# Optimization experiments

Measured on AMD Instinct MI355X. Metric: run time of the kernel, lower is better.

The kernel has to match this reference:

```python
import jax, jax.numpy as jnp
import numpy as np

B, CIN, H, W = 32, 512, 16, 16
COUT, HEADS, SPARSITY = 2048, 8, 7
D = COUT // HEADS  # 256, must equal H*W
N = H * W


def conv1x1(x, w, b):
    # x: [B,C,H,W], w: [O,C], b: [O]
    return jnp.einsum('bchw,oc->bohw', x, w) + b[None, :, None, None]


def setup_inputs() -> dict:
    key = jax.random.key(0)
    ks = jax.random.split(key, 11)
    def lin(k, o, c):
        bound = 1.0 / np.sqrt(c)
        kw, kb = jax.random.split(k)
        return (jax.random.uniform(kw, (o, c), jnp.float32, -bound, bound),
                jax.random.uniform(kb, (o,), jnp.float32, -bound, bound))
    Wq, bq = lin(ks[0], COUT, CIN)
    Wk, bk = lin(ks[1], COUT, CIN)
    Wv, bv = lin(ks[2], COUT, CIN)
    Wo, bo = lin(ks[3], COUT, COUT)
    # kaiming_uniform_ on [COUT, COUT]
    gain = np.sqrt(2.0) / np.sqrt(5.0)  # default a=sqrt(5)
    bound = gain * np.sqrt(3.0 / COUT)
    coeff = jax.random.uniform(ks[4], (COUT, COUT), jnp.float32, -bound, bound)
    scale = jnp.array([np.sqrt(D)], jnp.float32)
    x = jax.random.normal(ks[5], (B, CIN, H, W), jnp.float32)
    return {"x": x, "Wq": Wq, "bq": bq, "Wk": Wk, "bk": bk, "Wv": Wv,
            "bv": bv, "Wo": Wo, "bo": bo, "coeff": coeff, "scale": scale}


def reference(x, Wq, bq, Wk, bk, Wv, bv, Wo, bo, coeff, scale):
    # enforce_sparsity: keep top-`SPARSITY` |coeff| per row, zero the rest
    _, idx = jax.lax.top_k(jnp.abs(coeff), SPARSITY)  # [COUT, SPARSITY]
    mask = jnp.zeros(coeff.shape, bool).at[jnp.arange(COUT)[:, None], idx].set(True)
    coeff_s = jnp.where(mask, coeff, 0.0)

    q = conv1x1(x, Wq, bq).reshape(B, HEADS, D, N)
    k = conv1x1(x, Wk, bk).reshape(B, HEADS, D, N)
    v = conv1x1(x, Wv, bv).reshape(B, HEADS, D, N)

    attn = jnp.einsum('bhdn,bhdm->bhnm', q, k) / scale[0]  # [B,h,N,N]
    sparse_attn = jnp.einsum('bhnm,mp->bhnp', attn, coeff_s[:D, :D])
    sparse_attn = jax.nn.softmax(sparse_attn, axis=-1)
    out = jnp.einsum('bhnm,bhmd->bhnd', sparse_attn, v.transpose(0, 1, 3, 2))
    out = out.transpose(0, 1, 3, 2).reshape(B, COUT, H, W)
    return conv1x1(out, Wo, bo)
```

## Files before the change

kernel.cpp:

```cpp
#include <hip/hip_runtime.h>

typedef unsigned short ushort;
typedef __attribute__((ext_vector_type(8))) short short8;
typedef __attribute__((ext_vector_type(8))) unsigned short ushort8;
typedef __attribute__((ext_vector_type(4))) unsigned short ushort4v;
typedef __attribute__((ext_vector_type(4))) float fx4;

#define MAXNNZ (256*7)

__device__ __forceinline__ ushort f2bf(float f) {
    union { float f; unsigned u; } v; v.f = f;
    unsigned r = v.u + 0x7fffu + ((v.u >> 16) & 1u);
    return (ushort)(r >> 16);
}

__device__ __forceinline__ float bf2f(ushort b) {
    union { unsigned u; float f; } v; v.u = ((unsigned)b) << 16;
    return v.f;
}

__device__ __forceinline__ void gload_lds16(const ushort* g, ushort* l) {
    __builtin_amdgcn_global_load_lds(
        (const __attribute__((address_space(1))) unsigned int*)g,
        (__attribute__((address_space(3))) unsigned int*)l, 16, 0, 0);
}

__global__ __launch_bounds__(256)
void topk_kernel(const float* __restrict__ coeff,
                 int* __restrict__ coo_cnt, int* __restrict__ coo_m,
                 int* __restrict__ coo_p, float* __restrict__ coo_v)
{
    int row = blockIdx.x;
    int tid = threadIdx.x;
    const float* crow = coeff + (long)row * 2048;
    float av[8];
#pragma unroll
    for (int i = 0; i < 8; ++i) av[i] = fabsf(crow[tid + 256 * i]);
    __shared__ unsigned long long red[256];
    for (int t = 0; t < 7; ++t) {
        float mx = -1.f; int mi = 0;
#pragma unroll
        for (int i = 0; i < 8; ++i) if (av[i] > mx) { mx = av[i]; mi = i; }
        unsigned col = (unsigned)(tid + 256 * mi);
        unsigned long long pk = ((unsigned long long)__float_as_uint(mx) << 32)
                              | (unsigned long long)(2048u - col);
        red[tid] = pk; __syncthreads();
        for (int s = 128; s > 0; s >>= 1) {
            if (tid < s) { if (red[tid + s] > red[tid]) red[tid] = red[tid + s]; }
            __syncthreads();
        }
        unsigned long long w = red[0];
        __syncthreads();
        unsigned wcol = 2048u - (unsigned)(w & 0xffffffffu);
        if ((wcol & 255u) == (unsigned)tid) av[wcol >> 8] = -1.f;
        if (tid == 0 && wcol < 256u) {
            int pos = atomicAdd(coo_cnt, 1);
            coo_m[pos] = row; coo_p[pos] = (int)wcol; coo_v[pos] = crow[wcol];
        }
    }
}

__global__ __launch_bounds__(256)
void csc_kernel(const int* __restrict__ coo_cnt, const int* __restrict__ coo_m,
                const int* __restrict__ coo_p, const float* __restrict__ coo_v,
                int* __restrict__ csc_ptr, int* __restrict__ csc_m, float* __restrict__ csc_v)
{
    __shared__ int cnt[256];
    __shared__ int off[257];
    __shared__ int cur[256];
    int tid = threadIdx.x;
    cnt[tid] = 0;
    __syncthreads();
    int n = *coo_cnt; if (n > MAXNNZ) n = MAXNNZ;
    for (int e = tid; e < n; e += 256) atomicAdd(&cnt[coo_p[e]], 1);
    __syncthreads();
    if (tid == 0) {
        int s = 0;
        for (int p = 0; p < 256; ++p) { off[p] = s; s += cnt[p]; }
        off[256] = s;
    }
    __syncthreads();
    csc_ptr[tid] = off[tid];
    if (tid == 0) csc_ptr[256] = off[256];
    cur[tid] = off[tid];
    __syncthreads();
    for (int e = tid; e < n; e += 256) {
        int p = coo_p[e];
        int pos = atomicAdd(&cur[p], 1);
        csc_m[pos] = coo_m[e];
        csc_v[pos] = coo_v[e];
    }
}

__global__ void cvt4_kernel(const float* a0, ushort* d0, int n0,
                            const float* a1, ushort* d1, int n1,
                            const float* a2, ushort* d2, int n2,
                            const float* a3, ushort* d3, int n3)
{
    const float* s; ushort* d; int n;
    switch (blockIdx.y) {
        case 0: s = a0; d = d0; n = n0; break;
        case 1: s = a1; d = d1; n = n1; break;
        case 2: s = a2; d = d2; n = n2; break;
        default: s = a3; d = d3; n = n3; break;
    }
    int nv = n >> 2;
    for (int i = blockIdx.x * blockDim.x + threadIdx.x; i < nv; i += gridDim.x * blockDim.x) {
        fx4 v = ((const fx4*)s)[i];
        ushort4v o;
        o[0] = f2bf(v[0]); o[1] = f2bf(v[1]); o[2] = f2bf(v[2]); o[3] = f2bf(v[3]);
        ((ushort4v*)d)[i] = o;
    }
}

__global__ __launch_bounds__(256)
void transpose_f32_bf16(const float* __restrict__ in, ushort* __restrict__ out, int R, int C)
{
    int z = blockIdx.z;
    const float* ib = in + (long)z * R * C;
    ushort* ob = out + (long)z * R * C;
    __shared__ ushort tile[64][72];
    int r0 = blockIdx.x * 64, c0 = blockIdx.y * 64;
    int tid = threadIdx.x;
    int rl = tid >> 2, sg = tid & 3;
#pragma unroll
    for (int h = 0; h < 4; ++h) {
        fx4 v = *(const fx4*)(ib + (long)(r0 + rl) * C + c0 + h * 16 + sg * 4);
#pragma unroll
        for (int i = 0; i < 4; ++i) tile[h * 16 + sg * 4 + i][rl] = f2bf(v[i]);
    }
    __syncthreads();
    int cl = rl;
#pragma unroll
    for (int h = 0; h < 2; ++h) {
        ushort8 vv = *(const ushort8*)(&tile[cl][h * 32 + sg * 8]);
        *(ushort8*)(ob + (long)(c0 + cl) * R + r0 + h * 32 + sg * 8) = vv;
    }
}

__global__ __launch_bounds__(256)
void kcomb_kernel(const ushort* __restrict__ kbT, ushort* __restrict__ ktc,
                  const int* __restrict__ csc_ptr, const int* __restrict__ csc_m,
                  const float* __restrict__ csc_v)
{
    int z = blockIdx.y;
    int tid = threadIdx.x;
    int p = blockIdx.x * 64 + (tid >> 2);
    int d0 = (tid & 3) * 64;
    const ushort* src = kbT + (long)z * 65536;
    float acc[64];
#pragma unroll
    for (int i = 0; i < 64; ++i) acc[i] = 0.f;
    int e0 = csc_ptr[p], e1 = csc_ptr[p + 1];
    for (int e = e0; e < e1; ++e) {
        const ushort* row = src + csc_m[e] * 256 + d0;
        float c = csc_v[e];
#pragma unroll
        for (int u = 0; u < 8; ++u) {
            ushort8 v = *(const ushort8*)(row + u * 8);
#pragma unroll
            for (int t = 0; t < 8; ++t) acc[u * 8 + t] += bf2f(v[t]) * c;
        }
    }
    ushort* dst = ktc + (long)z * 65536 + (long)p * 256 + d0;
#pragma unroll
    for (int u = 0; u < 8; ++u) {
        ushort8 o;
#pragma unroll
        for (int t = 0; t < 8; ++t) o[t] = f2bf(acc[u * 8 + t]);
        *(ushort8*)(dst + u * 8) = o;
    }
}

template<int MODE>
__global__ __launch_bounds__(256)
void gemm128(const ushort* __restrict__ A, long long strideA,
             const ushort* __restrict__ B, long long strideB,
             void* __restrict__ C,
             const float* __restrict__ bias0, const float* __restrict__ bias1,
             const float* __restrict__ bias2,
             int N, int K)
{
    int z = blockIdx.z;
    const ushort* Ab = A + (long long)z * strideA;
    const ushort* Bb = B + (long long)z * strideB;
    int m0 = blockIdx.x * 128, n0 = blockIdx.y * 128;

    __shared__ __align__(16) ushort As[128 * 32];
    __shared__ __align__(16) ushort Bs[128 * 32];
    __shared__ __align__(16) ushort Ct[(MODE == 3) ? 128 * 136 : 8];

    int tid = threadIdx.x;
    int wave = tid >> 6, lane = tid & 63;
    int wrow = wave >> 1, wcol = wave & 1;
    int l16 = lane & 15, quad = lane >> 4;
    int lrow = lane >> 2, lkq = lane & 3;

    fx4 acc[4][4];
#pragma unroll
    for (int i = 0; i < 4; ++i)
#pragma unroll
        for (int j = 0; j < 4; ++j) acc[i][j] = (fx4){0.f, 0.f, 0.f, 0.f};

    const ushort* gA0 = Ab + (long)(m0 + wave * 16 + lrow) * K + lkq * 8;
    const ushort* gA1 = gA0 + (long)64 * K;
    const ushort* gB0 = Bb + (long)(n0 + wave * 16 + lrow) * K + lkq * 8;
    const ushort* gB1 = gB0 + (long)64 * K;
    ushort* lA0 = As + (wave * 16) * 32;
    ushort* lA1 = As + (64 + wave * 16) * 32;
    ushort* lB0 = Bs + (wave * 16) * 32;
    ushort* lB1 = Bs + (64 + wave * 16) * 32;

    for (int kc = 0; kc < K; kc += 32) {
        __syncthreads();
        gload_lds16(gA0 + kc, lA0);
        gload_lds16(gA1 + kc, lA1);
        gload_lds16(gB0 + kc, lB0);
        gload_lds16(gB1 + kc, lB1);
        __syncthreads();

        short8 af[4], bf[4];
#pragma unroll
        for (int i = 0; i < 4; ++i)
            af[i] = *(const short8*)(As + (wrow * 64 + i * 16 + l16) * 32 + quad * 8);
#pragma unroll
        for (int j = 0; j < 4; ++j)
            bf[j] = *(const short8*)(Bs + (wcol * 64 + j * 16 + l16) * 32 + quad * 8);
#pragma unroll
        for (int i = 0; i < 4; ++i)
#pragma unroll
            for (int j = 0; j < 4; ++j)
                acc[i][j] = __builtin_amdgcn_mfma_f32_16x16x32_bf16(af[i], bf[j], acc[i][j], 0, 0, 0);
    }

    if (MODE == 3) {
#pragma unroll
        for (int i = 0; i < 4; ++i)
#pragma unroll
            for (int j = 0; j < 4; ++j) {
                int ml = wrow * 64 + i * 16 + quad * 4;
                int nl = wcol * 64 + j * 16 + l16;
                ushort4v pk;
#pragma unroll
                for (int r = 0; r < 4; ++r) pk[r] = f2bf(acc[i][j][r]);
                *(ushort4v*)(Ct + nl * 136 + ml) = pk;
            }
        __syncthreads();
        long long zb = z >> 3; int zh = z & 7;
        int nl = tid >> 3, mc = (tid & 7) * 16;
#pragma unroll
        for (int p4 = 0; p4 < 4; ++p4) {
            int n = p4 * 32 + nl;
            ushort8 v0 = *(const ushort8*)(Ct + n * 136 + mc);
            ushort8 v1 = *(const ushort8*)(Ct + n * 136 + mc + 8);
            ushort* dst = (ushort*)C + zb * 524288 + (long)(n0 + n) * 2048
                        + zh * 256 + m0 + mc;
            *(ushort8*)dst = v0;
            *(ushort8*)(dst + 8) = v1;
        }
        return;
    }
}

template<int MODE>
__global__ __launch_bounds__(512, 2)
void gemm256(const ushort* __restrict__ A, const ushort* __restrict__ B,
             void* __restrict__ C,
             const float* __restrict__ bias0, const float* __restrict__ bias1,
             const float* __restrict__ bias2,
             int MT, int K)
{
    __shared__ __align__(16) ushort lds[4][2][8192];

    int nwg = gridDim.x;
    int bid = blockIdx.x;
    int cpx = nwg >> 3;
    int swz = (bid & 7) * cpx + (bid >> 3);
    int mt = swz % MT, nt = swz / MT;
    int m0 = mt << 8, n0 = nt << 8;

    int tid = threadIdx.x;
    int wave = tid >> 6, lane = tid & 63;
    int wr = wave >> 2, wc = wave & 3;
    int l16 = lane & 15, quad = lane >> 4;

    const ushort* gA0 = A + (long long)(m0 + wave * 16 + (lane >> 2)) * K + (lane & 3) * 8;
    const ushort* gA1 = gA0 + (long long)128 * K;
    const ushort* gB0 = B + (long long)(n0 + wave * 16 + (lane >> 2)) * K + (lane & 3) * 8;
    const ushort* gB1 = gB0 + (long long)128 * K;
    int ldso = wave * 512;

    fx4 acc[8][4];
#pragma unroll
    for (int i = 0; i < 8; ++i)
#pragma unroll
        for (int j = 0; j < 4; ++j) acc[i][j] = (fx4){0.f, 0.f, 0.f, 0.f};

    auto stage = [&](int b, int kc) {
        gload_lds16(gA0 + kc, &lds[b][0][ldso]);
        gload_lds16(gA1 + kc, &lds[b][0][4096 + ldso]);
        gload_lds16(gB0 + kc, &lds[b][1][ldso]);
        gload_lds16(gB1 + kc, &lds[b][1][4096 + ldso]);
    };
    auto compute = [&](int b) {
        short8 af[8], bf[4];
#pragma unroll
        for (int i = 0; i < 8; ++i)
            af[i] = *(const short8*)(&lds[b][0][(wr * 128 + i * 16 + l16) * 32 + quad * 8]);
#pragma unroll
        for (int j = 0; j < 4; ++j)
            bf[j] = *(const short8*)(&lds[b][1][(wc * 64 + j * 16 + l16) * 32 + quad * 8]);
        __builtin_amdgcn_s_setprio(1);
#pragma unroll
        for (int i = 0; i < 8; ++i)
#pragma unroll
            for (int j = 0; j < 4; ++j)
                acc[i][j] = __builtin_amdgcn_mfma_f32_16x16x32_bf16(af[i], bf[j], acc[i][j], 0, 0, 0);
        __builtin_amdgcn_s_setprio(0);
    };

    int NT = K >> 5;
    stage(0, 0); stage(1, 32); stage(2, 64);
    int kt = 0;
    for (; kt + 3 < NT; ++kt) {
        stage((kt + 3) & 3, (kt + 3) << 5);
        asm volatile("s_waitcnt vmcnt(12)" ::: "memory");
        __builtin_amdgcn_s_barrier();
        asm volatile("" ::: "memory");
        compute(kt & 3);
        asm volatile("" ::: "memory");
        __builtin_amdgcn_s_barrier();
    }
    asm volatile("s_waitcnt vmcnt(8)" ::: "memory");
    __builtin_amdgcn_s_barrier();
    asm volatile("" ::: "memory");
    compute(kt & 3); ++kt;
    asm volatile("" ::: "memory");
    __builtin_amdgcn_s_barrier();
    asm volatile("s_waitcnt vmcnt(4)" ::: "memory");
    __builtin_amdgcn_s_barrier();
    asm volatile("" ::: "memory");
    compute(kt & 3); ++kt;
    asm volatile("" ::: "memory");
    __builtin_amdgcn_s_barrier();
    asm volatile("s_waitcnt vmcnt(0)" ::: "memory");
    __builtin_amdgcn_s_barrier();
    asm volatile("" ::: "memory");
    compute(kt & 3);
    __builtin_amdgcn_s_barrier();

    if (MODE == 5) {
        float* Cf = (float*)C + (long long)nt * 524288;
#pragma unroll
        for (int i = 0; i < 8; ++i) {
            int m = m0 + wr * 128 + i * 16 + quad * 4;
#pragma unroll
            for (int j = 0; j < 4; ++j) {
                int n = wc * 64 + j * 16 + l16;
                float* dst = Cf + (long long)m * 256 + n;
#pragma unroll
                for (int r = 0; r < 4; ++r)
                    dst[(long)r * 256] = acc[i][j][r] + bias0[m + r];
            }
        }
        return;
    }

    if (MODE == 4) {
        int sec = m0 >> 11;
        int ms0 = m0 & 2047;
        ushort* ct = &lds[0][0][0];
        if (sec < 2) {
            const float* bs = (sec == 0) ? bias0 : bias1;
            ushort* base = (ushort*)C + (long long)sec * 16777216
                         + (long long)nt * 524288 + (long long)(ms0 >> 8) * 65536;
#pragma unroll
            for (int hh = 0; hh < 2; ++hh) {
                if ((wc >> 1) == hh) {
#pragma unroll
                    for (int i = 0; i < 8; ++i)
#pragma unroll
                        for (int j = 0; j < 4; ++j) {
                            int nl = (wc & 1) * 64 + j * 16 + l16;
                            int ml = wr * 128 + i * 16 + quad * 4;
                            ushort4v pk;
#pragma unroll
                            for (int r = 0; r < 4; ++r)
                                pk[r] = f2bf(acc[i][j][r] + bs[ms0 + ml + r]);
                            *(ushort4v*)(ct + nl * 264 + ml) = pk;
                        }
                }
                __syncthreads();
                int row = tid & 127, c0 = (tid >> 7) * 64;
                ushort* dst = base + (long long)(hh * 128 + row) * 256 + c0;
                const ushort* src = ct + row * 264 + c0;
#pragma unroll
                for (int u = 0; u < 8; ++u)
                    *(ushort8*)(dst + u * 8) = *(const ushort8*)(src + u * 8);
                __syncthreads();
            }
        } else {
            ushort* base = (ushort*)C + 33554432LL + (long long)nt * 524288
                         + (long long)ms0 * 256;
#pragma unroll
            for (int hh = 0; hh < 2; ++hh) {
                if (wr == hh) {
#pragma unroll
                    for (int i = 0; i < 8; ++i)
#pragma unroll
                        for (int j = 0; j < 4; ++j) {
                            int nl = wc * 64 + j * 16 + l16;
                            int ml = i * 16 + quad * 4;
#pragma unroll
                            for (int r = 0; r < 4; ++r)
                                ct[(ml + r) * 264 + nl] =
                                    f2bf(acc[i][j][r] + bias2[ms0 + hh * 128 + ml + r]);
                        }
                }
                __syncthreads();
                int row = tid & 127, c0 = (tid >> 7) * 64;
                ushort* dst = base + (long long)(hh * 128 + row) * 256 + c0;
                const ushort* src = ct + row * 264 + c0;
#pragma unroll
                for (int u = 0; u < 8; ++u)
                    *(ushort8*)(dst + u * 8) = *(const ushort8*)(src + u * 8);
                __syncthreads();
            }
        }
        return;
    }
}

__global__ __launch_bounds__(256)
void tsm_kernel(const ushort* __restrict__ Q, const ushort* __restrict__ Kt,
                ushort* __restrict__ P, const float* __restrict__ scale_src)
{
    int z = blockIdx.y;
    const ushort* Ab = Q + (long)z * 65536;
    const ushort* Bb = Kt + (long)z * 65536;
    int n0 = blockIdx.x * 128;

    __shared__ __align__(16) ushort As[128 * 32];
    __shared__ __align__(16) ushort Bs[256 * 32];
    __shared__ float rmax[2][128];
    __shared__ float rsum[2][128];

    int tid = threadIdx.x;
    int wave = tid >> 6, lane = tid & 63;
    int wrow = wave >> 1, wcol = wave & 1;
    int l16 = lane & 15, quad = lane >> 4;
    int lrow = lane >> 2, lkq = lane & 3;

    fx4 acc[4][8];
#pragma unroll
    for (int i = 0; i < 4; ++i)
#pragma unroll
        for (int j = 0; j < 8; ++j) acc[i][j] = (fx4){0.f, 0.f, 0.f, 0.f};

    const ushort* gA0 = Ab + (long)(n0 + wave * 16 + lrow) * 256 + lkq * 8;
    const ushort* gA1 = gA0 + 64 * 256;
    const ushort* gB0 = Bb + (long)(wave * 16 + lrow) * 256 + lkq * 8;
    ushort* lA0 = As + (wave * 16) * 32;
    ushort* lA1 = As + (64 + wave * 16) * 32;
    ushort* lB0 = Bs + (wave * 16) * 32;

    for (int kc = 0; kc < 256; kc += 32) {
        __syncthreads();
        gload_lds16(gA0 + kc, lA0);
        gload_lds16(gA1 + kc, lA1);
        gload_lds16(gB0 + kc, lB0);
        gload_lds16(gB0 + 64 * 256 + kc, lB0 + 64 * 32);
        gload_lds16(gB0 + 128 * 256 + kc, lB0 + 128 * 32);
        gload_lds16(gB0 + 192 * 256 + kc, lB0 + 192 * 32);
        __syncthreads();

        short8 af[4], bf[8];
#pragma unroll
        for (int i = 0; i < 4; ++i)
            af[i] = *(const short8*)(As + (wrow * 64 + i * 16 + l16) * 32 + quad * 8);
#pragma unroll
        for (int j = 0; j < 8; ++j)
            bf[j] = *(const short8*)(Bs + (wcol * 128 + j * 16 + l16) * 32 + quad * 8);
#pragma unroll
        for (int i = 0; i < 4; ++i)
#pragma unroll
            for (int j = 0; j < 8; ++j)
                acc[i][j] = __builtin_amdgcn_mfma_f32_16x16x32_bf16(af[i], bf[j], acc[i][j], 0, 0, 0);
    }

    float sc = 1.0f / scale_src[0];
#pragma unroll
    for (int i = 0; i < 4; ++i)
#pragma unroll
        for (int j = 0; j < 8; ++j)
#pragma unroll
            for (int r = 0; r < 4; ++r) acc[i][j][r] *= sc;

    float lm[4][4];
#pragma unroll
    for (int i = 0; i < 4; ++i)
#pragma unroll
        for (int r = 0; r < 4; ++r) {
            float m = -1e30f;
#pragma unroll
            for (int j = 0; j < 8; ++j) m = fmaxf(m, acc[i][j][r]);
            lm[i][r] = m;
        }
#pragma unroll
    for (int d = 1; d < 16; d <<= 1)
#pragma unroll
        for (int i = 0; i < 4; ++i)
#pragma unroll
            for (int r = 0; r < 4; ++r) lm[i][r] = fmaxf(lm[i][r], __shfl_xor(lm[i][r], d, 16));
    if (l16 == 0) {
#pragma unroll
        for (int i = 0; i < 4; ++i)
#pragma unroll
            for (int r = 0; r < 4; ++r)
                rmax[wcol][wrow * 64 + i * 16 + quad * 4 + r] = lm[i][r];
    }
    __syncthreads();

    float ls[4][4];
#pragma unroll
    for (int i = 0; i < 4; ++i)
#pragma unroll
        for (int r = 0; r < 4; ++r) {
            int row = wrow * 64 + i * 16 + quad * 4 + r;
            float M = fmaxf(rmax[0][row], rmax[1][row]);
            float s = 0.f;
#pragma unroll
            for (int j = 0; j < 8; ++j) {
                float e = __expf(acc[i][j][r] - M);
                acc[i][j][r] = e;
                s += e;
            }
            ls[i][r] = s;
        }
#pragma unroll
    for (int d = 1; d < 16; d <<= 1)
#pragma unroll
        for (int i = 0; i < 4; ++i)
#pragma unroll
            for (int r = 0; r < 4; ++r) ls[i][r] += __shfl_xor(ls[i][r], d, 16);
    if (l16 == 0) {
#pragma unroll
        for (int i = 0; i < 4; ++i)
#pragma unroll
            for (int r = 0; r < 4; ++r)
                rsum[wcol][wrow * 64 + i * 16 + quad * 4 + r] = ls[i][r];
    }
    __syncthreads();

    ushort* Pb = P + (long)z * 65536;
#pragma unroll
    for (int i = 0; i < 4; ++i)
#pragma unroll
        for (int r = 0; r < 4; ++r) {
            int row = wrow * 64 + i * 16 + quad * 4 + r;
            float inv = 1.0f / (rsum[0][row] + rsum[1][row]);
#pragma unroll
            for (int j = 0; j < 8; ++j)
                Pb[(long)(n0 + row) * 256 + wcol * 128 + j * 16 + l16] = f2bf(acc[i][j][r] * inv);
        }
}

extern "C" void kernel_launch(void* const* d_in, const int* in_sizes, int n_in,
                              void* d_out, int out_size, void* d_ws, size_t ws_size,
                              hipStream_t stream)
{
    const float* x     = (const float*)d_in[0];
    const float* Wq    = (const float*)d_in[1];
    const float* bq    = (const float*)d_in[2];
    const float* Wk    = (const float*)d_in[3];
    const float* bk    = (const float*)d_in[4];
    const float* Wv    = (const float*)d_in[5];
    const float* bv    = (const float*)d_in[6];
    const float* Wo    = (const float*)d_in[7];
    const float* bo    = (const float*)d_in[8];
    const float* coeff = (const float*)d_in[9];
    const float* scale = (const float*)d_in[10];
    float* out = (float*)d_out;

    size_t o = 0;
    char* w = (char*)d_ws;
    auto take = [&](size_t bytes) -> void* {
        void* p = w + o; o += (bytes + 255) & ~(size_t)255; return p;
    };
    int*    coo_cnt = (int*)take(4);
    int*    coo_m   = (int*)take(MAXNNZ * 4);
    int*    coo_p   = (int*)take(MAXNNZ * 4);
    float*  coo_v   = (float*)take(MAXNNZ * 4);
    int*    csc_ptr = (int*)take(257 * 4);
    int*    csc_m   = (int*)take(MAXNNZ * 4);
    float*  csc_v   = (float*)take(MAXNNZ * 4);
    ushort* wqkv = (ushort*)take(6144L * 512 * 2);
    ushort* wob  = (ushort*)take(2048L * 2048 * 2);
    ushort* xT   = (ushort*)take(32L * 256 * 512 * 2);
    ushort* qkv  = (ushort*)take(3 * 16777216L * 2);
    ushort* qbT = qkv;
    ushort* kbT = qkv + 16777216L;
    ushort* vb  = qkv + 33554432L;
    ushort* ktc = (ushort*)take(16777216L * 2);
    ushort* P_ws = kbT;
    ushort* obT  = qbT;
    (void)in_sizes; (void)n_in; (void)out_size; (void)ws_size;

    hipMemsetAsync(coo_cnt, 0, 4, stream);
    topk_kernel<<<256, 256, 0, stream>>>(coeff, coo_cnt, coo_m, coo_p, coo_v);
    csc_kernel<<<1, 256, 0, stream>>>(coo_cnt, coo_m, coo_p, coo_v, csc_ptr, csc_m, csc_v);

    cvt4_kernel<<<dim3(1024, 4, 1), 256, 0, stream>>>(
        Wq, wqkv, 2048 * 512, Wk, wqkv + 2048L * 512, 2048 * 512,
        Wv, wqkv + 4096L * 512, 2048 * 512, Wo, wob, 2048 * 2048);
    transpose_f32_bf16<<<dim3(8, 4, 32), 256, 0, stream>>>(x, xT, 512, 256);

    gemm256<4><<<dim3(768, 1, 1), dim3(512, 1, 1), 0, stream>>>(
        wqkv, xT, qkv, bq, bk, bv, 24, 512);

    kcomb_kernel<<<dim3(4, 256), 256, 0, stream>>>(kbT, ktc, csc_ptr, csc_m, csc_v);

    tsm_kernel<<<dim3(2, 256), 256, 0, stream>>>(qbT, ktc, P_ws, scale);

    gemm128<3><<<dim3(2, 2, 256), 256, 0, stream>>>(
        vb, 65536, P_ws, 65536, obT, nullptr, nullptr, nullptr, 256, 256);

    gemm256<5><<<dim3(256, 1, 1), dim3(512, 1, 1), 0, stream>>>(
        wob, obT, out, bo, nullptr, nullptr, 8, 2048);
}
```

Before: 397.7 us.

## Swizzle GEMM LDS layout and split k-step into two interleaved half-phases

Applies an XOR swizzle to the column offset of global-to-LDS loads and the matching fragment reads, aimed at removing LDS bank conflicts on the ds_read_b128 fragment loads. Restructures the main loop so each k-tile is computed in two halves of the A fragments, with A and B prefetch stages issued separately between the halves. This interleaves LDS reads, global prefetch and MFMA work and halves A-fragment register pressure. In exchange it adds more barriers per k-step and relies on hand-tuned vmcnt counts that must match the split stage issue order.

```diff
diff --git a/kernel.cpp b/kernel.cpp
--- a/kernel.cpp
+++ b/kernel.cpp
@@ -284,70 +284,85 @@
     int wr = wave >> 2, wc = wave & 3;
     int l16 = lane & 15, quad = lane >> 4;
 
-    const ushort* gA0 = A + (long long)(m0 + wave * 16 + (lane >> 2)) * K + (lane & 3) * 8;
+    int lc = (((lane & 3) ^ ((lane >> 3) & 3))) * 8;
+    const ushort* gA0 = A + (long long)(m0 + wave * 16 + (lane >> 2)) * K + lc;
     const ushort* gA1 = gA0 + (long long)128 * K;
-    const ushort* gB0 = B + (long long)(n0 + wave * 16 + (lane >> 2)) * K + (lane & 3) * 8;
+    const ushort* gB0 = B + (long long)(n0 + wave * 16 + (lane >> 2)) * K + lc;
     const ushort* gB1 = gB0 + (long long)128 * K;
     int ldso = wave * 512;
 
+    int rsw = ((l16 >> 1) & 3) * 8;
+    int aoff = (wr * 128 + l16) * 32 + ((quad * 8) ^ rsw);
+    int boff = (wc * 64 + l16) * 32 + ((quad * 8) ^ rsw);
+
     fx4 acc[8][4];
 #pragma unroll
     for (int i = 0; i < 8; ++i)
 #pragma unroll
         for (int j = 0; j < 4; ++j) acc[i][j] = (fx4){0.f, 0.f, 0.f, 0.f};
 
-    auto stage = [&](int b, int kc) {
+    auto stageA = [&](int b, int kc) {
         gload_lds16(gA0 + kc, &lds[b][0][ldso]);
         gload_lds16(gA1 + kc, &lds[b][0][4096 + ldso]);
+    };
+    auto stageB = [&](int b, int kc) {
         gload_lds16(gB0 + kc, &lds[b][1][ldso]);
         gload_lds16(gB1 + kc, &lds[b][1][4096 + ldso]);
     };
-    auto compute = [&](int b) {
-        short8 af[8], bf[4];
-#pragma unroll
-        for (int i = 0; i < 8; ++i)
-            af[i] = *(const short8*)(&lds[b][0][(wr * 128 + i * 16 + l16) * 32 + quad * 8]);
-#pragma unroll
-        for (int j = 0; j < 4; ++j)
-            bf[j] = *(const short8*)(&lds[b][1][(wc * 64 + j * 16 + l16) * 32 + quad * 8]);
+
+    short8 af[4], bf[4];
+    auto readA = [&](int b, int half) {
+        const ushort* p = &lds[b][0][aoff + half * 2048];
+#pragma unroll
+        for (int i = 0; i < 4; ++i) af[i] = *(const short8*)(p + i * 512);
+    };
+    auto readB = [&](int b) {
+        const ushort* p = &lds[b][1][boff];
+#pragma unroll
+        for (int j = 0; j < 4; ++j) bf[j] = *(const short8*)(p + j * 512);
+    };
+    auto mma = [&](int half) {
         __builtin_amdgcn_s_setprio(1);
 #pragma unroll
-        for (int i = 0; i < 8; ++i)
+        for (int i = 0; i < 4; ++i)
 #pragma unroll
             for (int j = 0; j < 4; ++j)
-                acc[i][j] = __builtin_amdgcn_mfma_f32_16x16x32_bf16(af[i], bf[j], acc[i][j], 0, 0, 0);
+                acc[half * 4 + i][j] =
+                    __builtin_amdgcn_mfma_f32_16x16x32_bf16(af[i], bf[j], acc[half * 4 + i][j], 0, 0, 0);
         __builtin_amdgcn_s_setprio(0);
     };
 
     int NT = K >> 5;
-    stage(0, 0); stage(1, 32); stage(2, 64);
-    int kt = 0;
-    for (; kt + 3 < NT; ++kt) {
-        stage((kt + 3) & 3, (kt + 3) << 5);
-        asm volatile("s_waitcnt vmcnt(12)" ::: "memory");
-        __builtin_amdgcn_s_barrier();
-        asm volatile("" ::: "memory");
-        compute(kt & 3);
-        asm volatile("" ::: "memory");
-        __builtin_amdgcn_s_barrier();
-    }
+    stageA(0, 0);  stageB(0, 0);
+    stageA(1, 32); stageB(1, 32);
+    stageA(2, 64); stageB(2, 64);
     asm volatile("s_waitcnt vmcnt(8)" ::: "memory");
     __builtin_amdgcn_s_barrier();
-    asm volatile("" ::: "memory");
-    compute(kt & 3); ++kt;
-    asm volatile("" ::: "memory");
-    __builtin_amdgcn_s_barrier();
-    asm volatile("s_waitcnt vmcnt(4)" ::: "memory");
-    __builtin_amdgcn_s_barrier();
-    asm volatile("" ::: "memory");
-    compute(kt & 3); ++kt;
-    asm volatile("" ::: "memory");
-    __builtin_amdgcn_s_barrier();
-    asm volatile("s_waitcnt vmcnt(0)" ::: "memory");
-    __builtin_amdgcn_s_barrier();
-    asm volatile("" ::: "memory");
-    compute(kt & 3);
-    __builtin_amdgcn_s_barrier();
+
+    for (int t = 0; t < NT; ++t) {
+        int b = t & 3;
+        readA(b, 0); readB(b);
+        if (t + 3 < NT) stageA((t + 3) & 3, (t + 3) << 5);
+        __builtin_amdgcn_s_barrier();
+        asm volatile("s_waitcnt lgkmcnt(0)" ::: "memory");
+        __builtin_amdgcn_sched_barrier(0);
+        mma(0);
+        __builtin_amdgcn_s_barrier();
+        readA(b, 1);
+        if (t + 3 < NT) {
+            stageB((t + 3) & 3, (t + 3) << 5);
+            asm volatile("s_waitcnt vmcnt(8)" ::: "memory");
+        } else if (t + 2 < NT) {
+            asm volatile("s_waitcnt vmcnt(4)" ::: "memory");
+        } else if (t + 1 < NT) {
+            asm volatile("s_waitcnt vmcnt(0)" ::: "memory");
+        }
+        __builtin_amdgcn_s_barrier();
+        asm volatile("s_waitcnt lgkmcnt(0)" ::: "memory");
+        __builtin_amdgcn_sched_barrier(0);
+        mma(1);
+        __builtin_amdgcn_s_barrier();
+    }
 
     if (MODE == 5) {
         float* Cf = (float*)C + (long long)nt * 524288;
```

Measured after the change: 386.3 us. 2.9% less time.
